# Optimization experiments

Measured on AMD Instinct MI355X. Metric: run time of the kernel, lower is better.

The kernel has to match this reference:

```python
import jax, jax.numpy as jnp
import numpy as np
import math

B, N, M, D = 8, 2048, 2048, 512

def setup_inputs() -> dict:
    key = jax.random.key(0)
    ks = jax.random.split(key, 12)
    s = 1.0 / math.sqrt(D)
    return {
        "query_xyz": jax.random.normal(ks[0], (B, N, 3), jnp.float32),
        "query_feat": jax.random.normal(ks[1], (B, N, D), jnp.float32),
        "key_xyz": jax.random.normal(ks[2], (B, M, 3), jnp.float32),
        "key_feat": jax.random.normal(ks[3], (B, M, D), jnp.float32),
        "Wq": jax.random.normal(ks[4], (D, D), jnp.float32) * s,
        "bq": jnp.zeros((D,), jnp.float32),
        "Wk": jax.random.normal(ks[5], (D, D), jnp.float32) * s,
        "bk": jnp.zeros((D,), jnp.float32),
        "Wv": jax.random.normal(ks[6], (D, D), jnp.float32) * s,
        "bv": jnp.zeros((D,), jnp.float32),
        "Wo": jax.random.normal(ks[7], (D, D), jnp.float32) * s,
        "bo": jnp.zeros((D,), jnp.float32),
        "ln_g": jnp.ones((D,), jnp.float32),
        "ln_b": jnp.zeros((D,), jnp.float32),
    }

def reference(query_xyz, query_feat, key_xyz, key_feat,
              Wq, bq, Wk, bk, Wv, bv, Wo, bo, ln_g, ln_b):
    d = query_feat.shape[-1]
    # projections (torch Linear: x @ W.T + b)
    Q = jnp.einsum('bnd,ed->bne', query_feat, Wq) + bq
    K = jnp.einsum('bmd,ed->bme', key_feat, Wk) + bk
    V = jnp.einsum('bmd,ed->bme', key_feat, Wv) + bv
    scores = jnp.einsum('bnd,bmd->bnm', Q, K) / jnp.sqrt(jnp.float32(d))
    # pairwise euclidean distance via (||q||^2 + ||k||^2 - 2 q.k), avoids BxNxMx3
    qn = jnp.sum(query_xyz * query_xyz, axis=-1)  # [B,N]
    kn = jnp.sum(key_xyz * key_xyz, axis=-1)      # [B,M]
    d2 = qn[:, :, None] + kn[:, None, :] - 2.0 * jnp.einsum('bnc,bmc->bnm', query_xyz, key_xyz)
    dist = jnp.sqrt(jnp.maximum(d2, 1e-12))
    # distance bias: log(exp(-2*dist) + 1e-8)
    scores = scores + jnp.log(jnp.exp(-dist * 2.0) + 1e-8)
    attn = jax.nn.softmax(scores, axis=-1)
    # dropout is identity in eval mode
    attended = jnp.einsum('bnm,bme->bne', attn, V)
    out = jnp.einsum('bne,fe->bnf', attended, Wo) + bo
    x = query_feat + out
    # LayerNorm (eps=1e-5)
    mu = jnp.mean(x, axis=-1, keepdims=True)
    var = jnp.mean((x - mu) ** 2, axis=-1, keepdims=True)
    return (x - mu) * jax.lax.rsqrt(var + 1e-5) * ln_g + ln_b
```

## Files before the change

kernel.cpp:

```cpp
#include <hip/hip_runtime.h>

typedef __attribute__((ext_vector_type(8))) short short8;
typedef __attribute__((ext_vector_type(8))) unsigned short us8;
typedef __attribute__((ext_vector_type(4))) unsigned short us4;
typedef __attribute__((ext_vector_type(4))) float f32x4;

__device__ __forceinline__ float bf2f(unsigned short h) {
  return __uint_as_float(((unsigned int)h) << 16);
}
__device__ __forceinline__ unsigned short f2bf(float f) {
  unsigned int u = __float_as_uint(f);
  u += 0x7FFF + ((u >> 16) & 1);
  return (unsigned short)(u >> 16);
}

__device__ __forceinline__ void gload16(const void* g, void* l) {
  __builtin_amdgcn_global_load_lds(
      (const __attribute__((address_space(1))) unsigned int*)g,
      (__attribute__((address_space(3))) unsigned int*)l, 16, 0, 0);
}

#define BM 128
#define BN 128
#define BK 32

struct EpiParams {
  const float* bias;
  const float* aux0;
  const float* aux1;
  const void*  aux2;
  long  saux;
  float scale;
};

template<int EPI>
__global__ __launch_bounds__(256)
void gemm_bt(const unsigned short* __restrict__ A, const unsigned short* __restrict__ B,
             void* __restrict__ Cout, int Kd, int lda, int ldb, int ldc,
             long sA, long sB, long sC, EpiParams ep)
{
  __shared__ __attribute__((aligned(16))) char smem[16384];
  char* Al = smem;
  char* Bl = smem + 8192;

  const int t    = threadIdx.x;
  const int lane = t & 63;
  const int wid  = t >> 6;
  const int wr   = wid >> 1;
  const int wc   = wid & 1;
  const int tr   = lane & 15;
  const int tg   = lane >> 4;

  const int bz    = blockIdx.z;
  const int rbase = blockIdx.y * BM;
  const int cbase = blockIdx.x * BN;

  const unsigned short* Ab = A + (long)bz * sA;
  const unsigned short* Bb = B + (long)bz * sB;
  const char* Asrc = (const char*)(Ab + (long)rbase * lda);
  const char* Bsrc = (const char*)(Bb + (long)cbase * ldb);
  const long lda_b = (long)lda * 2;
  const long ldb_b = (long)ldb * 2;

  f32x4 acc[4][4] = {};

  for (int k0 = 0; k0 < Kd; k0 += BK) {
#pragma unroll
    for (int it = 0; it < 2; ++it) {
      const int boff = (it * 4 + wid) * 1024 + lane * 16;
      const int r  = boff >> 6;
      const int cb = boff & 63;
      gload16(Asrc + (long)r * lda_b + (k0 * 2 + cb), Al + (it * 4 + wid) * 1024);
      gload16(Bsrc + (long)r * ldb_b + (k0 * 2 + cb), Bl + (it * 4 + wid) * 1024);
    }
    __syncthreads();

    short8 af[4], bf[4];
#pragma unroll
    for (int m = 0; m < 4; ++m)
      af[m] = *(const short8*)(Al + ((wr * 64 + m * 16 + tr) * 32 + tg * 8) * 2);
#pragma unroll
    for (int n = 0; n < 4; ++n)
      bf[n] = *(const short8*)(Bl + ((wc * 64 + n * 16 + tr) * 32 + tg * 8) * 2);
#pragma unroll
    for (int m = 0; m < 4; ++m)
#pragma unroll
      for (int n = 0; n < 4; ++n)
        acc[m][n] = __builtin_amdgcn_mfma_f32_16x16x32_bf16(af[m], bf[n], acc[m][n], 0, 0, 0);
    __syncthreads();
  }

  if (EPI == 0) {
    unsigned short* C = (unsigned short*)Cout + (long)bz * sC;
#pragma unroll
    for (int n = 0; n < 4; ++n) {
      const int col = cbase + wc * 64 + n * 16 + tr;
      const float bv = ep.bias ? ep.bias[col] : 0.f;
#pragma unroll
      for (int m = 0; m < 4; ++m) {
#pragma unroll
        for (int i = 0; i < 4; ++i) {
          const int row = rbase + wr * 64 + m * 16 + tg * 4 + i;
          C[(long)row * ldc + col] = f2bf(acc[m][n][i] + bv);
        }
      }
    }
  } else if (EPI == 4) {
    if (cbase < 512) {
      unsigned short* C = (unsigned short*)Cout;
#pragma unroll
      for (int n = 0; n < 4; ++n) {
        const int col = cbase + wc * 64 + n * 16 + tr;
        const float bv = ep.bias[col];
#pragma unroll
        for (int m = 0; m < 4; ++m) {
#pragma unroll
          for (int i = 0; i < 4; ++i) {
            const int row = rbase + wr * 64 + m * 16 + tg * 4 + i;
            C[(long)row * 512 + col] = f2bf(acc[m][n][i] + bv);
          }
        }
      }
    } else {
      unsigned short* C = (unsigned short*)ep.aux2;
#pragma unroll
      for (int n = 0; n < 4; ++n) {
        const int e  = cbase - 512 + wc * 64 + n * 16 + tr;
        const float bv = ep.aux1[e];
#pragma unroll
        for (int m = 0; m < 4; ++m) {
          const int row0 = rbase + wr * 64 + m * 16 + tg * 4;
          const int b  = row0 >> 11;
          const int ml = row0 & 2047;
          us4 v;
#pragma unroll
          for (int i = 0; i < 4; ++i) v[i] = f2bf(acc[m][n][i] + bv);
          *(us4*)(C + ((long)b * 512 + e) * 2048 + ml) = v;
        }
      }
    }
  } else {
    float* C = (float*)Cout;
    const float* qf = ep.aux0;
#pragma unroll
    for (int n = 0; n < 4; ++n) {
      const int col = cbase + wc * 64 + n * 16 + tr;
      const float bv = ep.bias ? ep.bias[col] : 0.f;
#pragma unroll
      for (int m = 0; m < 4; ++m) {
#pragma unroll
        for (int i = 0; i < 4; ++i) {
          const int row = rbase + wr * 64 + m * 16 + tg * 4 + i;
          C[(long)row * 512 + col] = acc[m][n][i] + bv + qf[(long)row * 512 + col];
        }
      }
    }
  }
}

template<int EPI>
__global__ __launch_bounds__(512, 2)
void gemm2(const unsigned short* __restrict__ A, const unsigned short* __restrict__ B,
           void* __restrict__ Cout, int Kd, int lda, int ldb, int ldc,
           long sA, long sB, long sC, int ntn, EpiParams ep)
{
  __shared__ __attribute__((aligned(16))) char smem[98304];

  const int t    = threadIdx.x;
  const int lane = t & 63;
  const int wid  = t >> 6;
  const int wr   = wid >> 2;
  const int wc   = wid & 3;
  const int tr   = lane & 15;
  const int tg   = lane >> 4;

  const int bz    = blockIdx.x;
  const int rbase = (blockIdx.y / ntn) * 128;
  const int cbase = (blockIdx.y % ntn) * 256;

  const long lda_b = (long)lda * 2;
  const long ldb_b = (long)ldb * 2;
  const char* Asrc = (const char*)(A + (long)bz * sA + (long)rbase * lda);
  const char* Bsrc = (const char*)(B + (long)bz * sB + (long)cbase * ldb);

  const int srow   = t >> 3;
  const int scol16 = (t & 7) ^ ((t >> 3) & 7);
  const char* gA[2];
  const char* gB[4];
#pragma unroll
  for (int c = 0; c < 2; ++c)
    gA[c] = Asrc + (long)(c * 64 + srow) * lda_b + scol16 * 16;
#pragma unroll
  for (int c = 0; c < 4; ++c)
    gB[c] = Bsrc + (long)(c * 64 + srow) * ldb_b + scol16 * 16;

  f32x4 acc[4][4] = {};
  const int NT = Kd >> 6;
  int slot = 0;

#pragma unroll
  for (int c = 0; c < 2; ++c) gload16(gA[c], smem + c * 8192 + wid * 1024);
#pragma unroll
  for (int c = 0; c < 4; ++c) gload16(gB[c], smem + 16384 + c * 8192 + wid * 1024);
  __syncthreads();

  for (int tk = 0; tk < NT; ++tk) {
    if (tk + 1 < NT) {
      const int so = (slot ^ 1) * 49152;
      const long adv = (long)(tk + 1) * 128;
#pragma unroll
      for (int c = 0; c < 2; ++c) gload16(gA[c] + adv, smem + so + c * 8192 + wid * 1024);
#pragma unroll
      for (int c = 0; c < 4; ++c) gload16(gB[c] + adv, smem + so + 16384 + c * 8192 + wid * 1024);
    }
    const char* As = smem + slot * 49152;
    const char* Bs = As + 16384;
    const int x7 = tr & 7;
#pragma unroll
    for (int ks = 0; ks < 2; ++ks) {
      const int coff = ((ks * 4 + tg) ^ x7) * 16;
      short8 af[4], bf[4];
#pragma unroll
      for (int m = 0; m < 4; ++m)
        af[m] = *(const short8*)(As + (wr * 64 + m * 16 + tr) * 128 + coff);
#pragma unroll
      for (int n = 0; n < 4; ++n)
        bf[n] = *(const short8*)(Bs + (wc * 64 + n * 16 + tr) * 128 + coff);
#pragma unroll
      for (int m = 0; m < 4; ++m)
#pragma unroll
        for (int n = 0; n < 4; ++n)
          acc[m][n] = __builtin_amdgcn_mfma_f32_16x16x32_bf16(af[m], bf[n], acc[m][n], 0, 0, 0);
    }
    __syncthreads();
    slot ^= 1;
  }

  if (EPI == 0) {
    unsigned short* C = (unsigned short*)Cout + (long)bz * sC;
    const float* ls = (const float*)ep.aux2 + (long)bz * 2048 + rbase + wr * 64;
#pragma unroll
    for (int m = 0; m < 4; ++m) {
      const f32x4 lv = *(const f32x4*)(ls + m * 16 + tg * 4);
      f32x4 inv;
#pragma unroll
      for (int i = 0; i < 4; ++i) inv[i] = 1.f / lv[i];
#pragma unroll
      for (int n = 0; n < 4; ++n) {
        const int col = cbase + wc * 64 + n * 16 + tr;
#pragma unroll
        for (int i = 0; i < 4; ++i) {
          const int row = rbase + wr * 64 + m * 16 + tg * 4 + i;
          C[(long)row * ldc + col] = f2bf(acc[m][n][i] * inv[i]);
        }
      }
    }
  } else {
    float* qs  = (float*)smem;
    float* ks2 = (float*)smem + 384;
    if (t < 128) {
      const float* q = ep.aux0 + (long)bz * ep.saux + (long)(rbase + t) * 3;
      qs[t * 3] = q[0]; qs[t * 3 + 1] = q[1]; qs[t * 3 + 2] = q[2];
    } else if (t < 384) {
      const int tt = t - 128;
      const float* k2 = ep.aux1 + (long)bz * ep.saux + (long)(cbase + tt) * 3;
      ks2[tt * 3] = k2[0]; ks2[tt * 3 + 1] = k2[1]; ks2[tt * 3 + 2] = k2[2];
    }
    __syncthreads();
    unsigned short* C = (unsigned short*)Cout + (long)bz * sC;
    float* lrow = (float*)ep.aux2 + (long)bz * 2048 + rbase;
    float ps[4][4];
#pragma unroll
    for (int m = 0; m < 4; ++m) {
#pragma unroll
      for (int i = 0; i < 4; ++i) {
        ps[m][i] = 0.f;
        const int rl = wr * 64 + m * 16 + tg * 4 + i;
        const float qx = qs[rl * 3], qy = qs[rl * 3 + 1], qz = qs[rl * 3 + 2];
#pragma unroll
        for (int n = 0; n < 4; ++n) {
          const int cl = wc * 64 + n * 16 + tr;
          const float dx = qx - ks2[cl * 3];
          const float dy = qy - ks2[cl * 3 + 1];
          const float dz = qz - ks2[cl * 3 + 2];
          const float d2 = dx * dx + dy * dy + dz * dz;
          const float d  = sqrtf(fmaxf(d2, 1e-12f));
          const float bias = fmaxf(-2.f * d, -18.420680743952367f);
          const float p = __expf(acc[m][n][i] * ep.scale + bias - 5.f);
          ps[m][i] += p;
          C[(long)(rbase + rl) * ldc + (cbase + cl)] = f2bf(p);
        }
      }
    }
#pragma unroll
    for (int off = 1; off <= 8; off <<= 1)
#pragma unroll
      for (int m = 0; m < 4; ++m)
#pragma unroll
        for (int i = 0; i < 4; ++i)
          ps[m][i] += __shfl_xor(ps[m][i], off, 64);
    if (tr == 0) {
#pragma unroll
      for (int m = 0; m < 4; ++m)
#pragma unroll
        for (int i = 0; i < 4; ++i)
          atomicAdd(&lrow[wr * 64 + m * 16 + tg * 4 + i], ps[m][i]);
    }
  }
}

__global__ __launch_bounds__(256)
void ln_rows(const float* __restrict__ X, const float* __restrict__ g,
             const float* __restrict__ b, float* __restrict__ O)
{
  const int row  = blockIdx.x * 4 + (threadIdx.x >> 6);
  const int lane = threadIdx.x & 63;
  const float* xp = X + (long)row * 512;

  f32x4 v0 = *(const f32x4*)(xp + lane * 4);
  f32x4 v1 = *(const f32x4*)(xp + 256 + lane * 4);

  float s = 0.f;
#pragma unroll
  for (int j = 0; j < 4; ++j) s += v0[j] + v1[j];
#pragma unroll
  for (int off = 32; off; off >>= 1) s += __shfl_xor(s, off, 64);
  const float mu = s * (1.f / 512.f);

  float vs = 0.f;
#pragma unroll
  for (int j = 0; j < 4; ++j) {
    float d0 = v0[j] - mu, d1 = v1[j] - mu;
    vs += d0 * d0 + d1 * d1;
  }
#pragma unroll
  for (int off = 32; off; off >>= 1) vs += __shfl_xor(vs, off, 64);
  const float r = rsqrtf(vs * (1.f / 512.f) + 1e-5f);

  f32x4 g0 = *(const f32x4*)(g + lane * 4);
  f32x4 g1 = *(const f32x4*)(g + 256 + lane * 4);
  f32x4 b0 = *(const f32x4*)(b + lane * 4);
  f32x4 b1 = *(const f32x4*)(b + 256 + lane * 4);

  f32x4 o0, o1;
#pragma unroll
  for (int j = 0; j < 4; ++j) {
    o0[j] = (v0[j] - mu) * r * g0[j] + b0[j];
    o1[j] = (v1[j] - mu) * r * g1[j] + b1[j];
  }
  float* op = O + (long)row * 512;
  *(f32x4*)(op + lane * 4) = o0;
  *(f32x4*)(op + 256 + lane * 4) = o1;
}

__global__ __launch_bounds__(256)
void cvt_feat(const float* __restrict__ a, const float* __restrict__ b,
              unsigned short* __restrict__ oa, unsigned short* __restrict__ ob)
{
  const float* src = blockIdx.y ? b : a;
  unsigned short* dst = blockIdx.y ? ob : oa;
  const long i = blockIdx.x * 256 + threadIdx.x;
  const f32x4* s = (const f32x4*)src;
  f32x4 x = s[i * 2];
  f32x4 y = s[i * 2 + 1];
  us8 o;
#pragma unroll
  for (int j = 0; j < 4; ++j) { o[j] = f2bf(x[j]); o[4 + j] = f2bf(y[j]); }
  *(us8*)(dst + i * 8) = o;
}

__global__ __launch_bounds__(256)
void cvt_w(const float* __restrict__ w0, const float* __restrict__ w1,
           const float* __restrict__ w2, const float* __restrict__ w3,
           unsigned short* __restrict__ dst)
{
  const float* src = blockIdx.y == 0 ? w0 : blockIdx.y == 1 ? w1 : blockIdx.y == 2 ? w2 : w3;
  unsigned short* d = dst + (long)blockIdx.y * 262144;
  const long i = blockIdx.x * 256 + threadIdx.x;
  const f32x4* s = (const f32x4*)src;
  f32x4 x = s[i * 2];
  f32x4 y = s[i * 2 + 1];
  us8 o;
#pragma unroll
  for (int j = 0; j < 4; ++j) { o[j] = f2bf(x[j]); o[4 + j] = f2bf(y[j]); }
  *(us8*)(d + i * 8) = o;
}

extern "C" void kernel_launch(void* const* d_in, const int* in_sizes, int n_in,
                              void* d_out, int out_size, void* d_ws, size_t ws_size,
                              hipStream_t stream)
{
  const float* qxyz  = (const float*)d_in[0];
  const float* qfeat = (const float*)d_in[1];
  const float* kxyz  = (const float*)d_in[2];
  const float* kfeat = (const float*)d_in[3];
  const float* Wq = (const float*)d_in[4];
  const float* bq = (const float*)d_in[5];
  const float* Wk = (const float*)d_in[6];
  const float* bk = (const float*)d_in[7];
  const float* Wv = (const float*)d_in[8];
  const float* bv = (const float*)d_in[9];
  const float* Wo = (const float*)d_in[10];
  const float* bo = (const float*)d_in[11];
  const float* lng = (const float*)d_in[12];
  const float* lnb = (const float*)d_in[13];

  const long SZ_FEAT = 16777216;
  char* ws = (char*)d_ws;
  if (ws_size < (size_t)153092096) return;

  unsigned short* XQ  = (unsigned short*)(ws);
  unsigned short* XK  = (unsigned short*)(ws + SZ_FEAT);
  unsigned short* QB  = (unsigned short*)(ws + 2 * SZ_FEAT);
  unsigned short* KB  = (unsigned short*)(ws + 3 * SZ_FEAT);
  unsigned short* VT  = (unsigned short*)(ws + 4 * SZ_FEAT);
  unsigned short* WQB = (unsigned short*)(ws + 5 * SZ_FEAT);
  unsigned short* WKB = WQB + 262144;
  unsigned short* WOB = WQB + 786432;
  unsigned short* SB  = (unsigned short*)(ws + 5 * SZ_FEAT + 2097152);
  unsigned short* ATT = QB;
  float* XRES = (float*)ws;
  float* LSUM = (float*)(ws + SZ_FEAT);

  cvt_feat<<<dim3(4096, 2), 256, 0, stream>>>(qfeat, kfeat, XQ, XK);
  cvt_w<<<dim3(128, 4), 256, 0, stream>>>(Wq, Wk, Wv, Wo, WQB);

  EpiParams e0{}; e0.bias = bq;
  gemm_bt<0><<<dim3(4, 128, 1), 256, 0, stream>>>(XQ, WQB, QB, 512, 512, 512, 512, 0, 0, 0, e0);
  EpiParams e1{}; e1.bias = bk; e1.aux1 = bv; e1.aux2 = VT;
  gemm_bt<4><<<dim3(8, 128, 1), 256, 0, stream>>>(XK, WKB, KB, 512, 512, 512, 512, 0, 0, 0, e1);

  hipMemsetAsync(LSUM, 0, 8 * 2048 * sizeof(float), stream);

  EpiParams es{}; es.aux0 = qxyz; es.aux1 = kxyz; es.aux2 = LSUM; es.saux = 2048 * 3;
  es.scale = 0.044194173824159216f;
  gemm2<2><<<dim3(8, 128), 512, 0, stream>>>(QB, KB, SB, 512, 512, 512, 2048,
                                             (long)2048 * 512, (long)2048 * 512,
                                             (long)2048 * 2048, 8, es);

  EpiParams ep{}; ep.aux2 = LSUM;
  gemm2<0><<<dim3(8, 32), 512, 0, stream>>>(SB, VT, ATT, 2048, 2048, 2048, 512,
                                            (long)2048 * 2048, (long)512 * 2048,
                                            (long)2048 * 512, 2, ep);

  EpiParams eo{}; eo.bias = bo; eo.aux0 = qfeat;
  gemm_bt<3><<<dim3(4, 128, 1), 256, 0, stream>>>(ATT, WOB, XRES, 512, 512, 512, 512, 0, 0, 0, eo);

  ln_rows<<<4096, 256, 0, stream>>>(XRES, lng, lnb, (float*)d_out);
}
```

Measured before the change: 261.5 us.

## Fold Wo into V projection and retile attention GEMMs to 128x128

Precomputes Wo·Wv and Wo·bv so the V projection directly yields output-space values, which removes the separate output projection GEMM; the PV GEMM epilogue now adds bo and the residual and writes fp32. Both attention GEMMs move from 512-thread 128x256 tiles to 256-thread 128x128 tiles with smaller LDS. MFMA sections are wrapped in s_setprio. Probabilities are staged through LDS so global stores are coalesced. The weight fold adds an extra bf16 rounding step and a few small setup kernels.

```diff
diff --git a/kernel.cpp b/kernel.cpp
--- a/kernel.cpp
+++ b/kernel.cpp
@@ -105,7 +105,7 @@
         }
       }
     }
-  } else if (EPI == 4) {
+  } else {
     if (cbase < 512) {
       unsigned short* C = (unsigned short*)Cout;
 #pragma unroll
@@ -139,81 +139,76 @@
         }
       }
     }
-  } else {
-    float* C = (float*)Cout;
-    const float* qf = ep.aux0;
-#pragma unroll
-    for (int n = 0; n < 4; ++n) {
-      const int col = cbase + wc * 64 + n * 16 + tr;
-      const float bv = ep.bias ? ep.bias[col] : 0.f;
-#pragma unroll
-      for (int m = 0; m < 4; ++m) {
-#pragma unroll
-        for (int i = 0; i < 4; ++i) {
-          const int row = rbase + wr * 64 + m * 16 + tg * 4 + i;
-          C[(long)row * 512 + col] = acc[m][n][i] + bv + qf[(long)row * 512 + col];
-        }
-      }
-    }
   }
 }
 
 template<int EPI>
-__global__ __launch_bounds__(512, 2)
-void gemm2(const unsigned short* __restrict__ A, const unsigned short* __restrict__ B,
-           void* __restrict__ Cout, int Kd, int lda, int ldb, int ldc,
-           long sA, long sB, long sC, int ntn, EpiParams ep)
-{
-  __shared__ __attribute__((aligned(16))) char smem[98304];
+__global__ __launch_bounds__(256, 2)
+void gemm128(const unsigned short* __restrict__ A, const unsigned short* __restrict__ B,
+             void* __restrict__ Cout, int Kd, int lda, int ldb, int ldc,
+             long sA, long sB, long sC, int ntn, EpiParams ep)
+{
+  __shared__ __attribute__((aligned(16))) char smem[68608];
 
   const int t    = threadIdx.x;
   const int lane = t & 63;
   const int wid  = t >> 6;
-  const int wr   = wid >> 2;
-  const int wc   = wid & 3;
+  const int wr   = wid >> 1;
+  const int wc   = wid & 1;
   const int tr   = lane & 15;
   const int tg   = lane >> 4;
 
   const int bz    = blockIdx.x;
   const int rbase = (blockIdx.y / ntn) * 128;
-  const int cbase = (blockIdx.y % ntn) * 256;
+  const int cbase = (blockIdx.y % ntn) * 128;
 
   const long lda_b = (long)lda * 2;
   const long ldb_b = (long)ldb * 2;
   const char* Asrc = (const char*)(A + (long)bz * sA + (long)rbase * lda);
   const char* Bsrc = (const char*)(B + (long)bz * sB + (long)cbase * ldb);
 
-  const int srow   = t >> 3;
-  const int scol16 = (t & 7) ^ ((t >> 3) & 7);
-  const char* gA[2];
+  const int srow = t >> 3;
+  const int sg   = (t & 7) ^ ((t >> 3) & 7);
+  const char* gA[4];
   const char* gB[4];
 #pragma unroll
-  for (int c = 0; c < 2; ++c)
-    gA[c] = Asrc + (long)(c * 64 + srow) * lda_b + scol16 * 16;
-#pragma unroll
-  for (int c = 0; c < 4; ++c)
-    gB[c] = Bsrc + (long)(c * 64 + srow) * ldb_b + scol16 * 16;
+  for (int c = 0; c < 4; ++c) {
+    gA[c] = Asrc + (long)(c * 32 + srow) * lda_b + sg * 16;
+    gB[c] = Bsrc + (long)(c * 32 + srow) * ldb_b + sg * 16;
+  }
+
+  if (EPI == 2) {
+    float* qs  = (float*)(smem + 65536);
+    float* ks2 = (float*)(smem + 65536 + 1536);
+    if (t < 128) {
+      const float* q = ep.aux0 + (long)bz * ep.saux + (long)(rbase + t) * 3;
+      qs[t * 3] = q[0]; qs[t * 3 + 1] = q[1]; qs[t * 3 + 2] = q[2];
+    } else {
+      const int tt = t - 128;
+      const float* k2 = ep.aux1 + (long)bz * ep.saux + (long)(cbase + tt) * 3;
+      ks2[tt * 3] = k2[0]; ks2[tt * 3 + 1] = k2[1]; ks2[tt * 3 + 2] = k2[2];
+    }
+  }
 
   f32x4 acc[4][4] = {};
   const int NT = Kd >> 6;
+
+#define STG(TK, S)                                                            \
+  {                                                                           \
+    char* _b = smem + (S) * 32768;                                            \
+    const long _adv = (long)(TK) * 128;                                       \
+    _Pragma("unroll")                                                         \
+    for (int c = 0; c < 4; ++c) gload16(gA[c] + _adv, _b + c * 4096 + wid * 1024); \
+    _Pragma("unroll")                                                         \
+    for (int c = 0; c < 4; ++c) gload16(gB[c] + _adv, _b + 16384 + c * 4096 + wid * 1024); \
+  }
+
+  STG(0, 0);
+  __syncthreads();
   int slot = 0;
-
-#pragma unroll
-  for (int c = 0; c < 2; ++c) gload16(gA[c], smem + c * 8192 + wid * 1024);
-#pragma unroll
-  for (int c = 0; c < 4; ++c) gload16(gB[c], smem + 16384 + c * 8192 + wid * 1024);
-  __syncthreads();
-
   for (int tk = 0; tk < NT; ++tk) {
-    if (tk + 1 < NT) {
-      const int so = (slot ^ 1) * 49152;
-      const long adv = (long)(tk + 1) * 128;
-#pragma unroll
-      for (int c = 0; c < 2; ++c) gload16(gA[c] + adv, smem + so + c * 8192 + wid * 1024);
-#pragma unroll
-      for (int c = 0; c < 4; ++c) gload16(gB[c] + adv, smem + so + 16384 + c * 8192 + wid * 1024);
-    }
-    const char* As = smem + slot * 49152;
+    if (tk + 1 < NT) STG(tk + 1, slot ^ 1);
+    const char* As = smem + slot * 32768;
     const char* Bs = As + 16384;
     const int x7 = tr & 7;
 #pragma unroll
@@ -226,19 +221,23 @@
 #pragma unroll
       for (int n = 0; n < 4; ++n)
         bf[n] = *(const short8*)(Bs + (wc * 64 + n * 16 + tr) * 128 + coff);
+      __builtin_amdgcn_s_setprio(1);
 #pragma unroll
       for (int m = 0; m < 4; ++m)
 #pragma unroll
         for (int n = 0; n < 4; ++n)
           acc[m][n] = __builtin_amdgcn_mfma_f32_16x16x32_bf16(af[m], bf[n], acc[m][n], 0, 0, 0);
+      __builtin_amdgcn_s_setprio(0);
     }
     __syncthreads();
     slot ^= 1;
   }
+#undef STG
 
   if (EPI == 0) {
-    unsigned short* C = (unsigned short*)Cout + (long)bz * sC;
+    float* C = (float*)Cout + (long)bz * sC;
     const float* ls = (const float*)ep.aux2 + (long)bz * 2048 + rbase + wr * 64;
+    const float* qf = ep.aux0;
 #pragma unroll
     for (int m = 0; m < 4; ++m) {
       const f32x4 lv = *(const f32x4*)(ls + m * 16 + tg * 4);
@@ -248,26 +247,19 @@
 #pragma unroll
       for (int n = 0; n < 4; ++n) {
         const int col = cbase + wc * 64 + n * 16 + tr;
+        const float bb = ep.bias[col];
 #pragma unroll
         for (int i = 0; i < 4; ++i) {
           const int row = rbase + wr * 64 + m * 16 + tg * 4 + i;
-          C[(long)row * ldc + col] = f2bf(acc[m][n][i] * inv[i]);
+          C[(long)row * ldc + col] =
+              acc[m][n][i] * inv[i] + bb + qf[((long)bz * 2048 + row) * 512 + col];
         }
       }
     }
   } else {
-    float* qs  = (float*)smem;
-    float* ks2 = (float*)smem + 384;
-    if (t < 128) {
-      const float* q = ep.aux0 + (long)bz * ep.saux + (long)(rbase + t) * 3;
-      qs[t * 3] = q[0]; qs[t * 3 + 1] = q[1]; qs[t * 3 + 2] = q[2];
-    } else if (t < 384) {
-      const int tt = t - 128;
-      const float* k2 = ep.aux1 + (long)bz * ep.saux + (long)(cbase + tt) * 3;
-      ks2[tt * 3] = k2[0]; ks2[tt * 3 + 1] = k2[1]; ks2[tt * 3 + 2] = k2[2];
-    }
-    __syncthreads();
-    unsigned short* C = (unsigned short*)Cout + (long)bz * sC;
+    const float* qs  = (const float*)(smem + 65536);
+    const float* ks2 = (const float*)(smem + 65536 + 1536);
+    unsigned short* sP = (unsigned short*)smem;
     float* lrow = (float*)ep.aux2 + (long)bz * 2048 + rbase;
     float ps[4][4];
 #pragma unroll
@@ -288,7 +280,7 @@
           const float bias = fmaxf(-2.f * d, -18.420680743952367f);
           const float p = __expf(acc[m][n][i] * ep.scale + bias - 5.f);
           ps[m][i] += p;
-          C[(long)(rbase + rl) * ldc + (cbase + cl)] = f2bf(p);
+          sP[rl * 136 + cl] = f2bf(p);
         }
       }
     }
@@ -305,6 +297,15 @@
 #pragma unroll
         for (int i = 0; i < 4; ++i)
           atomicAdd(&lrow[wr * 64 + m * 16 + tg * 4 + i], ps[m][i]);
+    }
+    __syncthreads();
+    unsigned short* C = (unsigned short*)Cout + (long)bz * sC + (long)rbase * ldc + cbase;
+#pragma unroll
+    for (int c = 0; c < 8; ++c) {
+      const int L = c * 256 + t;
+      const int row = L >> 4, g = L & 15;
+      const us8 v = *(const us8*)(sP + row * 136 + g * 8);
+      *(us8*)(C + (long)row * ldc + g * 8) = v;
     }
   }
 }
@@ -384,6 +385,45 @@
 #pragma unroll
   for (int j = 0; j < 4; ++j) { o[j] = f2bf(x[j]); o[4 + j] = f2bf(y[j]); }
   *(us8*)(d + i * 8) = o;
+}
+
+__global__ __launch_bounds__(256)
+void cvt_wT(const float* __restrict__ Wv, unsigned short* __restrict__ WvT)
+{
+  __shared__ float tile[64 * 68];
+  const int t = threadIdx.x;
+  const int e0 = blockIdx.y * 64, d0 = blockIdx.x * 64;
+#pragma unroll
+  for (int c = 0; c < 4; ++c) {
+    const int L = c * 256 + t;
+    const int r = L >> 4, g = L & 15;
+    const f32x4 v = *(const f32x4*)(Wv + (long)(e0 + r) * 512 + d0 + g * 4);
+    *(f32x4*)(tile + r * 68 + g * 4) = v;
+  }
+  __syncthreads();
+#pragma unroll
+  for (int c = 0; c < 2; ++c) {
+    const int L = c * 256 + t;
+    const int d = L >> 3, ge = L & 7;
+    us8 o;
+#pragma unroll
+    for (int j = 0; j < 8; ++j) o[j] = f2bf(tile[(ge * 8 + j) * 68 + d]);
+    *(us8*)(WvT + (long)(d0 + d) * 512 + e0 + ge * 8) = o;
+  }
+}
+
+__global__ __launch_bounds__(256)
+void bvo_k(const float* __restrict__ Wo, const float* __restrict__ bv,
+           float* __restrict__ out)
+{
+  const int f = blockIdx.x * 256 + threadIdx.x;
+  float s = 0.f;
+  for (int e = 0; e < 512; e += 4) {
+    const f32x4 w = *(const f32x4*)(Wo + (long)f * 512 + e);
+    const f32x4 b = *(const f32x4*)(bv + e);
+    s += w[0] * b[0] + w[1] * b[1] + w[2] * b[2] + w[3] * b[3];
+  }
+  out[f] = s;
 }
 
 extern "C" void kernel_launch(void* const* d_in, const int* in_sizes, int n_in,
@@ -416,35 +456,39 @@
   unsigned short* VT  = (unsigned short*)(ws + 4 * SZ_FEAT);
   unsigned short* WQB = (unsigned short*)(ws + 5 * SZ_FEAT);
   unsigned short* WKB = WQB + 262144;
+  unsigned short* WVO = WQB + 524288;
   unsigned short* WOB = WQB + 786432;
   unsigned short* SB  = (unsigned short*)(ws + 5 * SZ_FEAT + 2097152);
-  unsigned short* ATT = QB;
+  unsigned short* WVT = SB;
+  float* BVO  = (float*)((char*)SB + 524288);
   float* XRES = (float*)ws;
-  float* LSUM = (float*)(ws + SZ_FEAT);
+  float* LSUM = (float*)(WOB);
 
   cvt_feat<<<dim3(4096, 2), 256, 0, stream>>>(qfeat, kfeat, XQ, XK);
   cvt_w<<<dim3(128, 4), 256, 0, stream>>>(Wq, Wk, Wv, Wo, WQB);
+  cvt_wT<<<dim3(8, 8), 256, 0, stream>>>(Wv, WVT);
+  bvo_k<<<dim3(2), 256, 0, stream>>>(Wo, bv, BVO);
+
+  EpiParams ew{};
+  gemm_bt<0><<<dim3(4, 4, 1), 256, 0, stream>>>(WOB, WVT, WVO, 512, 512, 512, 512, 0, 0, 0, ew);
 
   EpiParams e0{}; e0.bias = bq;
   gemm_bt<0><<<dim3(4, 128, 1), 256, 0, stream>>>(XQ, WQB, QB, 512, 512, 512, 512, 0, 0, 0, e0);
-  EpiParams e1{}; e1.bias = bk; e1.aux1 = bv; e1.aux2 = VT;
+  EpiParams e1{}; e1.bias = bk; e1.aux1 = BVO; e1.aux2 = VT;
   gemm_bt<4><<<dim3(8, 128, 1), 256, 0, stream>>>(XK, WKB, KB, 512, 512, 512, 512, 0, 0, 0, e1);
 
   hipMemsetAsync(LSUM, 0, 8 * 2048 * sizeof(float), stream);
 
   EpiParams es{}; es.aux0 = qxyz; es.aux1 = kxyz; es.aux2 = LSUM; es.saux = 2048 * 3;
   es.scale = 0.044194173824159216f;
-  gemm2<2><<<dim3(8, 128), 512, 0, stream>>>(QB, KB, SB, 512, 512, 512, 2048,
-                                             (long)2048 * 512, (long)2048 * 512,
-                                             (long)2048 * 2048, 8, es);
-
-  EpiParams ep{}; ep.aux2 = LSUM;
-  gemm2<0><<<dim3(8, 32), 512, 0, stream>>>(SB, VT, ATT, 2048, 2048, 2048, 512,
-                                            (long)2048 * 2048, (long)512 * 2048,
-                                            (long)2048 * 512, 2, ep);
-
-  EpiParams eo{}; eo.bias = bo; eo.aux0 = qfeat;
-  gemm_bt<3><<<dim3(4, 128, 1), 256, 0, stream>>>(ATT, WOB, XRES, 512, 512, 512, 512, 0, 0, 0, eo);
+  gemm128<2><<<dim3(8, 256), 256, 0, stream>>>(QB, KB, SB, 512, 512, 512, 2048,
+                                               (long)2048 * 512, (long)2048 * 512,
+                                               (long)2048 * 2048, 16, es);
+
+  EpiParams ep{}; ep.aux2 = LSUM; ep.bias = bo; ep.aux0 = qfeat;
+  gemm128<0><<<dim3(8, 64), 256, 0, stream>>>(SB, VT, XRES, 2048, 2048, 2048, 512,
+                                              (long)2048 * 2048, (long)512 * 2048,
+                                              (long)2048 * 512, 4, ep);
 
   ln_rows<<<4096, 256, 0, stream>>>(XRES, lng, lnb, (float*)d_out);
 }
```

New measurement: 276.8 us. 5.8% more time.
